# Kernel optimization log

Measured on AMD Instinct MI355X. Metric: run time of the kernel, lower is better.

The kernel has to match this reference:

```python
import jax, jax.numpy as jnp
import numpy as np
from jax.scipy.special import digamma, gammaln, logsumexp

N, K, D = 262144, 256, 64
ALPHA = 1.0  # alphaDP
LOG2PI = float(np.log(2.0 * np.pi))


def setup_inputs() -> dict:
    key = jax.random.key(0)
    k1, k2, k3, k4 = jax.random.split(key, 4)
    x = jax.random.normal(k1, (N, D), jnp.float32)
    # variational params (perturbed from the module's init so grads are nontrivial)
    u = 1.0 + jax.random.uniform(k2, (K,), jnp.float32)
    v = 1.0 + jax.random.uniform(k3, (K,), jnp.float32)
    tau = jax.random.normal(k4, (K, D), jnp.float32)
    c = jnp.ones((K,), jnp.float32)
    n = jnp.full((K,), float(D), jnp.float32)   # must be > D-1
    B = jnp.ones((K, D), jnp.float32)
    # fixed prior hyper-parameters (buffers, per init_kwargs)
    tau0 = jnp.zeros((K, D), jnp.float32)
    c0 = jnp.ones((K,), jnp.float32)
    n0 = jnp.full((K,), float(D), jnp.float32)
    B0 = jnp.ones((K, D), jnp.float32)
    return dict(x=x, u=u, v=v, tau=tau, c=c, n=n, B=B,
                tau0=tau0, c0=c0, n0=n0, B0=B0)


def _dpmm_forward(x, u, v, tau, c, n, B, tau0, c0, n0, B0):
    # --- E[log pi_k] from stick-breaking Beta(u_k, v_k) posteriors ---
    dig_sum = digamma(u + v)
    elog_beta = digamma(u) - dig_sum            # (K,)
    elog_1mbeta = digamma(v) - dig_sum          # (K,)
    elog_pi = elog_beta + jnp.concatenate(
        [jnp.zeros((1,), elog_beta.dtype), jnp.cumsum(elog_1mbeta)[:-1]])

    # --- expected Gaussian log-likelihood under diagonal Normal-Wishart q ---
    Elam = n[:, None] / B                                        # (K, D) E[lambda]
    Eloglam = digamma(0.5 * n)[:, None] + jnp.log(2.0) - jnp.log(B)
    # quadratic form sum_d E[lam_kd](x_id - tau_kd)^2 via matmuls (no NxKxD tensor)
    quad = ((x * x) @ Elam.T
            - 2.0 * (x @ (Elam * tau).T)
            + jnp.sum(Elam * tau * tau, axis=-1)[None, :])       # (N, K)
    eloglik = 0.5 * (jnp.sum(Eloglam, axis=-1)[None, :]
                     - D * LOG2PI
                     - (D / c)[None, :]
                     - quad)                                     # (N, K)

    # --- responsibilities ---
    log_rho = elog_pi[None, :] + eloglik                         # (N, K)
    lse = logsumexp(log_rho, axis=-1)                            # (N,)
    pi = jnp.exp(log_rho - lse[:, None])                         # (N, K)

    # --- ELBO: sum_i r_ik (log_rho - log r) = sum_i logsumexp_i, minus KLs ---
    # KL(Beta(u,v) || Beta(1, alpha))
    kl_beta = jnp.sum(gammaln(u + v) - gammaln(u) - gammaln(v)
                      - (gammaln(1.0 + ALPHA) - gammaln(ALPHA))
                      + (u - 1.0) * elog_beta
                      + (v - ALPHA) * elog_1mbeta)
    # KL of diagonal Wishart (per-dim Gamma(n/2, rate=B/2))
    a, a0 = 0.5 * n[:, None], 0.5 * n0[:, None]
    b, b0 = 0.5 * B, 0.5 * B0
    kl_gam = ((a - a0) * digamma(a) - gammaln(a) + gammaln(a0)
              + a0 * (jnp.log(b) - jnp.log(b0)) + a * (b0 - b) / b)  # (K, D)
    # E_lambda KL of conditional Normal(tau, (c lambda)^-1)
    kl_norm = (0.5 * D * (c0 / c - 1.0 + jnp.log(c / c0))
               + 0.5 * c0 * jnp.sum((n[:, None] / B) * (tau - tau0) ** 2, axis=-1))

    elbo = jnp.sum(lse) - kl_beta - jnp.sum(kl_gam) - jnp.sum(kl_norm)
    return pi, elbo


def reference(x, u, v, tau, c, n, B, tau0, c0, n0, B0):
    return _dpmm_forward(x, u, v, tau, c, n, B, tau0, c0, n0, B0)
```

## Files before the change

### kernel.cpp

```cpp
#include <hip/hip_runtime.h>
#include <math.h>

#define NPTS 262144
#define KCL  256
#define DDIM 64
#define ALPHA_DP 1.0f

#define ROWS_PER_WAVE 32
#define WAVES_PER_BLK 4
#define ROWS_PER_BLK  (ROWS_PER_WAVE * WAVES_PER_BLK)
#define NBLK_MAIN     (NPTS / ROWS_PER_BLK)
#define NPART         (NPTS / ROWS_PER_WAVE)

#define OFF_ELOGPI 32768
#define OFF_BASE   33024
#define OFF_KLB    33280
#define OFF_KLP    33281
#define OFF_PART   33537

#define LN2_F    0.6931471805599453f
#define LOG2PI_F 1.8378770664093453f

typedef _Float16 f16x8  __attribute__((ext_vector_type(8)));
typedef float    f32x4  __attribute__((ext_vector_type(4)));
typedef float    f32x16 __attribute__((ext_vector_type(16)));

__device__ __forceinline__ float digamma_f(float x) {
  float r = 0.0f;
  while (x < 6.0f) { r -= 1.0f / x; x += 1.0f; }
  float inv  = 1.0f / x;
  float inv2 = inv * inv;
  return r + logf(x) - 0.5f * inv
       - inv2 * (0.083333333333333333f
         - inv2 * (0.008333333333333333f
           - inv2 * 0.003968253968253968f));
}

__global__ void dpmm_beta(const float* __restrict__ u, const float* __restrict__ v,
                          float* __restrict__ ws) {
  __shared__ float eb_s[KCL], e1b_s[KCL], klb_s[KCL];
  const int k = threadIdx.x;
  float uk = u[k], vk = v[k];
  float ds  = digamma_f(uk + vk);
  float eb  = digamma_f(uk) - ds;
  float e1b = digamma_f(vk) - ds;
  eb_s[k] = eb; e1b_s[k] = e1b;
  klb_s[k] = lgammaf(uk + vk) - lgammaf(uk) - lgammaf(vk)
           - (lgammaf(1.0f + ALPHA_DP) - lgammaf(ALPHA_DP))
           + (uk - 1.0f) * eb + (vk - ALPHA_DP) * e1b;
  __syncthreads();
  if (k == 0) {
    float run = 0.0f;
    for (int j = 0; j < KCL; ++j) { ws[OFF_ELOGPI + j] = eb_s[j] + run; run += e1b_s[j]; }
    double t = 0.0;
    for (int j = 0; j < KCL; ++j) t += (double)klb_s[j];
    ws[OFF_KLB] = (float)t;
  }
}

__global__ __launch_bounds__(64) void dpmm_w(
    const float* __restrict__ tau, const float* __restrict__ c,
    const float* __restrict__ n,   const float* __restrict__ B,
    const float* __restrict__ tau0, const float* __restrict__ c0,
    const float* __restrict__ n0,  const float* __restrict__ B0,
    float* __restrict__ ws) {
  const int k = blockIdx.x, d = threadIdx.x;
  _Float16* Wp = (_Float16*)ws;

  float nk = n[k], ck = c[k], n0k = n0[k], c0k = c0[k];
  float Bkd = B[k * DDIM + d],   tkd  = tau[k * DDIM + d];
  float B0kd = B0[k * DDIM + d], t0kd = tau0[k * DDIM + d];
  float Elam = nk / Bkd;
  float wb = Elam * tkd;
  float wa = -0.5f * Elam;

  const int ct = k & 7, col = k >> 3;
  int   kks[2] = { d, 64 + d };
  float wvs[2] = { wb, wa };
  #pragma unroll
  for (int q = 0; q < 2; ++q) {
    int kk = kks[q]; float wq = wvs[q];
    int s = kk >> 4, rem = kk & 15, h = rem >> 3, e = rem & 7;
    int lanei = col + h * 32;
    _Float16 hi = (_Float16)wq, lo = (_Float16)(wq - (float)hi);
    Wp[(( s * 8 + ct)      ) * 512 + lanei * 8 + e] = hi;
    Wp[((64 + s * 8 + ct)  ) * 512 + lanei * 8 + e] = lo;
  }

  float a = 0.5f * nk, a0 = 0.5f * n0k;
  float dga = digamma_f(a);
  float lga = lgammaf(a), lga0 = lgammaf(a0);
  float b = 0.5f * Bkd, b0 = 0.5f * B0kd;
  float klg = (a - a0) * dga - lga + lga0
            + a0 * (logf(b) - logf(b0)) + a * (b0 - b) / b;
  float dt = tkd - t0kd;
  float knq = Elam * dt * dt;
  float negLogB = -logf(Bkd);
  float et2 = Elam * tkd * tkd;

  #pragma unroll
  for (int off = 32; off; off >>= 1) {
    klg      += __shfl_xor(klg, off, 64);
    knq      += __shfl_xor(knq, off, 64);
    negLogB  += __shfl_xor(negLogB, off, 64);
    et2      += __shfl_xor(et2, off, 64);
  }
  if (d == 0) {
    float sumEloglam = (float)DDIM * (dga + LN2_F) + negLogB;
    ws[OFF_BASE + k] = ws[OFF_ELOGPI + k]
        + 0.5f * (sumEloglam - (float)DDIM * LOG2PI_F
                  - (float)DDIM / ck - et2);
    float kln = 0.5f * (float)DDIM * (c0k / ck - 1.0f + logf(ck / c0k))
              + 0.5f * c0k * knq;
    ws[OFF_KLP + k] = klg + kln;
  }
}

__device__ __forceinline__ void split8(const float* v, f16x8& h, f16x8& l) {
  #pragma unroll
  for (int e = 0; e < 8; ++e) {
    _Float16 hh = (_Float16)v[e];
    h[e] = hh;
    l[e] = (_Float16)(v[e] - (float)hh);
  }
}

__global__ __launch_bounds__(256, 2) void dpmm_mfma(
    const float* __restrict__ x, const _Float16* __restrict__ Wp,
    const float* __restrict__ base,
    float* __restrict__ pi, float* __restrict__ partial) {
  __shared__ _Float16 W_sh[2][8192];
  const int tid  = threadIdx.x;
  const int lane = tid & 63;
  const int w    = tid >> 6;
  const int col  = lane & 31;
  const int h    = lane >> 5;

  const long row0 = (long)blockIdx.x * ROWS_PER_BLK + (long)w * ROWS_PER_WAVE;
  const float* xr = x + (row0 + col) * DDIM + h * 8;
  float4 xa[4], xb[4];
  #pragma unroll
  for (int s = 0; s < 4; ++s) {
    xa[s] = *(const float4*)(xr + s * 16);
    xb[s] = *(const float4*)(xr + s * 16 + 4);
  }

  const f32x4* Wv = (const f32x4*)Wp;
  f32x4 st[4];
  #pragma unroll
  for (int i = 0; i < 4; ++i) st[i] = Wv[i * 256 + tid];

  f16x8 ah[8], al[8];
  #pragma unroll
  for (int s = 0; s < 4; ++s) {
    float cv[8] = {xa[s].x,xa[s].y,xa[s].z,xa[s].w,xb[s].x,xb[s].y,xb[s].z,xb[s].w};
    float qv[8];
    #pragma unroll
    for (int e = 0; e < 8; ++e) qv[e] = cv[e] * cv[e];
    split8(cv, ah[s], al[s]);
    split8(qv, ah[s + 4], al[s + 4]);
  }

  f32x16 acc[8];
  {
    float4 b0 = *(const float4*)(base + col * 8);
    float4 b1 = *(const float4*)(base + col * 8 + 4);
    float bb[8] = {b0.x,b0.y,b0.z,b0.w,b1.x,b1.y,b1.z,b1.w};
    #pragma unroll
    for (int ct = 0; ct < 8; ++ct) {
      #pragma unroll
      for (int j = 0; j < 16; ++j) acc[ct][j] = bb[ct];
    }
  }

  {
    f32x4* dst = (f32x4*)W_sh[0];
    #pragma unroll
    for (int i = 0; i < 4; ++i) dst[i * 256 + tid] = st[i];
    #pragma unroll
    for (int i = 0; i < 4; ++i) st[i] = Wv[1024 + i * 256 + tid];
  }
  __syncthreads();

  #pragma unroll
  for (int c = 0; c < 8; ++c) {
    const _Float16* Ws = W_sh[c & 1];
    #pragma unroll
    for (int f = 0; f < 16; ++f) {
      const int ct = f & 7;
      f16x8 b = *(const f16x8*)&Ws[f * 512 + lane * 8];
      if (c < 4) {
        const int s = 2 * c + (f >> 3);
        acc[ct] = __builtin_amdgcn_mfma_f32_32x32x16_f16(ah[s], b, acc[ct], 0, 0, 0);
        acc[ct] = __builtin_amdgcn_mfma_f32_32x32x16_f16(al[s], b, acc[ct], 0, 0, 0);
      } else {
        const int s = 2 * (c - 4) + (f >> 3);
        acc[ct] = __builtin_amdgcn_mfma_f32_32x32x16_f16(ah[s], b, acc[ct], 0, 0, 0);
      }
    }
    if (c < 7) {
      f32x4* dst = (f32x4*)W_sh[(c + 1) & 1];
      #pragma unroll
      for (int i = 0; i < 4; ++i) dst[i * 256 + tid] = st[i];
      if (c < 6) {
        #pragma unroll
        for (int i = 0; i < 4; ++i)
          st[i] = Wv[(size_t)(c + 2) * 1024 + i * 256 + tid];
      }
      __syncthreads();
    }
  }

  float wls = 0.0f;
  #pragma unroll
  for (int j = 0; j < 16; ++j) {
    const int r = (j & 3) + 8 * (j >> 2) + 4 * h;
    float m = acc[0][j];
    #pragma unroll
    for (int ct = 1; ct < 8; ++ct) m = fmaxf(m, acc[ct][j]);
    m = fmaxf(m, __shfl_xor(m, 1, 64));
    m = fmaxf(m, __shfl_xor(m, 2, 64));
    m = fmaxf(m, __shfl_xor(m, 4, 64));
    m = fmaxf(m, __shfl_xor(m, 8, 64));
    m = fmaxf(m, __shfl_xor(m, 16, 64));
    float ev[8]; float s = 0.0f;
    #pragma unroll
    for (int ct = 0; ct < 8; ++ct) { ev[ct] = __expf(acc[ct][j] - m); s += ev[ct]; }
    s += __shfl_xor(s, 1, 64);
    s += __shfl_xor(s, 2, 64);
    s += __shfl_xor(s, 4, 64);
    s += __shfl_xor(s, 8, 64);
    s += __shfl_xor(s, 16, 64);
    float rs = 1.0f / s;
    float* pr = pi + (size_t)(row0 + r) * KCL + col * 8;
    f32x4 p0 = { ev[0]*rs, ev[1]*rs, ev[2]*rs, ev[3]*rs };
    f32x4 p1 = { ev[4]*rs, ev[5]*rs, ev[6]*rs, ev[7]*rs };
    *(f32x4*)(pr + 0) = p0;
    *(f32x4*)(pr + 4) = p1;
    wls += m + __logf(s);
  }
  wls += __shfl_xor(wls, 1, 64);
  wls += __shfl_xor(wls, 2, 64);
  wls += __shfl_xor(wls, 4, 64);
  wls += __shfl_xor(wls, 8, 64);
  wls += __shfl_xor(wls, 16, 64);
  wls += __shfl_xor(wls, 32, 64);
  if (lane == 0) partial[blockIdx.x * WAVES_PER_BLK + w] = wls * 0.03125f;
}

__global__ void dpmm_fin(const float* __restrict__ ws,
                         float* __restrict__ out_elbo) {
  __shared__ double red[256];
  const int t = threadIdx.x;
  double s = 0.0;
  for (int i = t; i < NPART; i += 256) s += (double)ws[OFF_PART + i];
  s -= (double)ws[OFF_KLP + t];
  red[t] = s;
  __syncthreads();
  for (int off = 128; off; off >>= 1) {
    if (t < off) red[t] += red[t + off];
    __syncthreads();
  }
  if (t == 0) out_elbo[0] = (float)(red[0] - (double)ws[OFF_KLB]);
}

extern "C" void kernel_launch(void* const* d_in, const int* in_sizes, int n_in,
                              void* d_out, int out_size, void* d_ws, size_t ws_size,
                              hipStream_t stream) {
  const float* x    = (const float*)d_in[0];
  const float* u    = (const float*)d_in[1];
  const float* v    = (const float*)d_in[2];
  const float* tau  = (const float*)d_in[3];
  const float* c    = (const float*)d_in[4];
  const float* n    = (const float*)d_in[5];
  const float* B    = (const float*)d_in[6];
  const float* tau0 = (const float*)d_in[7];
  const float* c0   = (const float*)d_in[8];
  const float* n0   = (const float*)d_in[9];
  const float* B0   = (const float*)d_in[10];

  float* out = (float*)d_out;
  float* ws  = (float*)d_ws;

  dpmm_beta<<<1, KCL, 0, stream>>>(u, v, ws);
  dpmm_w<<<KCL, DDIM, 0, stream>>>(tau, c, n, B, tau0, c0, n0, B0, ws);

  const _Float16* Wp = (const _Float16*)ws;
  const float* base  = ws + OFF_BASE;
  float* partial     = ws + OFF_PART;

  dpmm_mfma<<<NBLK_MAIN, 256, 0, stream>>>(x, Wp, base, out, partial);
  dpmm_fin<<<1, 256, 0, stream>>>(ws, out + (size_t)NPTS * KCL);
}
```

Baseline: 120.5 us.

## Load weight tiles directly into LDS and halve pipeline stages

Replaces the register-staged weight copy (global load into VGPRs, then LDS store) with global_load_lds direct-to-LDS transfers. It also doubles each LDS buffer so the 8 chunk iterations become 4, which halves the number of block barriers. The aim is to free staging registers and VALU store work, and to cut synchronisation in the MFMA loop. In exchange the kernel uses twice the LDS per block, which could limit occupancy, and it depends on the compiler inserting correct waits for the asynchronous LDS writes.

New measurement: 117.5 us. 2.5% less time.

```diff
diff --git a/kernel.cpp b/kernel.cpp
--- a/kernel.cpp
+++ b/kernel.cpp
@@ -1,5 +1,6 @@
 #include <hip/hip_runtime.h>
 #include <math.h>
+#include <stdint.h>
 
 #define NPTS 262144
 #define KCL  256
@@ -125,11 +126,20 @@
   }
 }
 
+__device__ __forceinline__ void gload16(const _Float16* g, _Float16* l) {
+  __builtin_amdgcn_global_load_lds(
+      reinterpret_cast<const __attribute__((address_space(1))) uint32_t*>(
+          reinterpret_cast<uintptr_t>(g)),
+      reinterpret_cast<__attribute__((address_space(3))) uint32_t*>(
+          reinterpret_cast<uintptr_t>(l)),
+      16, 0, 0);
+}
+
 __global__ __launch_bounds__(256, 2) void dpmm_mfma(
     const float* __restrict__ x, const _Float16* __restrict__ Wp,
     const float* __restrict__ base,
     float* __restrict__ pi, float* __restrict__ partial) {
-  __shared__ _Float16 W_sh[2][8192];
+  __shared__ _Float16 W_sh[2][16384];
   const int tid  = threadIdx.x;
   const int lane = tid & 63;
   const int w    = tid >> 6;
@@ -145,10 +155,9 @@
     xb[s] = *(const float4*)(xr + s * 16 + 4);
   }
 
-  const f32x4* Wv = (const f32x4*)Wp;
-  f32x4 st[4];
-  #pragma unroll
-  for (int i = 0; i < 4; ++i) st[i] = Wv[i * 256 + tid];
+  #pragma unroll
+  for (int i = 0; i < 8; ++i)
+    gload16(Wp + (i * 256 + tid) * 8, &W_sh[0][(i * 256 + w * 64) * 8]);
 
   f16x8 ah[8], al[8];
   #pragma unroll
@@ -173,42 +182,34 @@
     }
   }
 
-  {
-    f32x4* dst = (f32x4*)W_sh[0];
-    #pragma unroll
-    for (int i = 0; i < 4; ++i) dst[i * 256 + tid] = st[i];
-    #pragma unroll
-    for (int i = 0; i < 4; ++i) st[i] = Wv[1024 + i * 256 + tid];
-  }
   __syncthreads();
 
   #pragma unroll
-  for (int c = 0; c < 8; ++c) {
+  for (int c = 0; c < 4; ++c) {
+    if (c + 1 < 4) {
+      #pragma unroll
+      for (int i = 0; i < 8; ++i)
+        gload16(Wp + (size_t)(c + 1) * 16384 + (i * 256 + tid) * 8,
+                &W_sh[(c + 1) & 1][(i * 256 + w * 64) * 8]);
+    }
     const _Float16* Ws = W_sh[c & 1];
     #pragma unroll
-    for (int f = 0; f < 16; ++f) {
-      const int ct = f & 7;
+    for (int f = 0; f < 32; ++f) {
+      const int ss = f >> 3, ct = f & 7;
       f16x8 b = *(const f16x8*)&Ws[f * 512 + lane * 8];
-      if (c < 4) {
-        const int s = 2 * c + (f >> 3);
-        acc[ct] = __builtin_amdgcn_mfma_f32_32x32x16_f16(ah[s], b, acc[ct], 0, 0, 0);
-        acc[ct] = __builtin_amdgcn_mfma_f32_32x32x16_f16(al[s], b, acc[ct], 0, 0, 0);
+      if (c == 0) {
+        acc[ct] = __builtin_amdgcn_mfma_f32_32x32x16_f16(ah[ss], b, acc[ct], 0, 0, 0);
+        acc[ct] = __builtin_amdgcn_mfma_f32_32x32x16_f16(al[ss], b, acc[ct], 0, 0, 0);
+      } else if (c == 1) {
+        acc[ct] = __builtin_amdgcn_mfma_f32_32x32x16_f16(ah[4 + ss], b, acc[ct], 0, 0, 0);
+        acc[ct] = __builtin_amdgcn_mfma_f32_32x32x16_f16(al[4 + ss], b, acc[ct], 0, 0, 0);
+      } else if (c == 2) {
+        acc[ct] = __builtin_amdgcn_mfma_f32_32x32x16_f16(ah[ss], b, acc[ct], 0, 0, 0);
       } else {
-        const int s = 2 * (c - 4) + (f >> 3);
-        acc[ct] = __builtin_amdgcn_mfma_f32_32x32x16_f16(ah[s], b, acc[ct], 0, 0, 0);
+        acc[ct] = __builtin_amdgcn_mfma_f32_32x32x16_f16(ah[4 + ss], b, acc[ct], 0, 0, 0);
       }
     }
-    if (c < 7) {
-      f32x4* dst = (f32x4*)W_sh[(c + 1) & 1];
-      #pragma unroll
-      for (int i = 0; i < 4; ++i) dst[i * 256 + tid] = st[i];
-      if (c < 6) {
-        #pragma unroll
-        for (int i = 0; i < 4; ++i)
-          st[i] = Wv[(size_t)(c + 2) * 1024 + i * 256 + tid];
-      }
-      __syncthreads();
-    }
+    if (c + 1 < 4) __syncthreads();
   }
 
   float wls = 0.0f;
```
